# Performance work log

Measured on AMD Instinct MI355X. Metric: run time of the kernel, lower is better.

Reference implementation:

```python
import jax, jax.numpy as jnp
import numpy as np

NUM_HEADS = 16
EMBED_DIM = 2048
HEAD_DIM = EMBED_DIM // NUM_HEADS        # 128
LATENT_DIM = HEAD_DIM // 4               # 32
GROUPS = HEAD_DIM // LATENT_DIM          # 4 latent sub-heads per q head
B, T = 1, 2048


def setup_inputs() -> dict:
    key = jax.random.key(0)
    ks = jax.random.split(key, 7)
    s_in = 1.0 / np.sqrt(EMBED_DIM)
    x = jax.random.normal(ks[0], (B, T, EMBED_DIM), dtype=jnp.float32)
    # torch Linear weights: [out_features, in_features]
    Wq = jax.random.normal(ks[1], (EMBED_DIM, EMBED_DIM), dtype=jnp.float32) * s_in
    Wk = jax.random.normal(ks[2], (EMBED_DIM, EMBED_DIM), dtype=jnp.float32) * s_in
    Wv = jax.random.normal(ks[3], (EMBED_DIM, EMBED_DIM), dtype=jnp.float32) * s_in
    Wlk = jax.random.normal(ks[4], (NUM_HEADS * LATENT_DIM, EMBED_DIM), dtype=jnp.float32) * s_in
    Wlv = jax.random.normal(ks[5], (NUM_HEADS * LATENT_DIM, EMBED_DIM), dtype=jnp.float32) * s_in
    Wo = jax.random.normal(ks[6], (EMBED_DIM, EMBED_DIM), dtype=jnp.float32) * s_in
    return {"x": x, "Wq": Wq, "Wk": Wk, "Wv": Wv, "Wlk": Wlk, "Wlv": Wlv, "Wo": Wo}


def reference(x, Wq, Wk, Wv, Wlk, Wlv, Wo):
    Bv, Tv, C = x.shape
    # q: [B,T,H,G,Dl]  (each head's 128-dim q split into 4 latent sub-heads)
    q = (x @ Wq.T).reshape(Bv, Tv, NUM_HEADS, GROUPS, LATENT_DIM)
    # latent k/v: [B,T,H,Dl], shared across the G sub-heads of each q head
    lk = (x @ Wlk.T).reshape(Bv, Tv, NUM_HEADS, LATENT_DIM)
    lv = (x @ Wlv.T).reshape(Bv, Tv, NUM_HEADS, LATENT_DIM)
    # k_proj / v_proj outputs are computed but unused in the original forward.
    scale = 1.0 / np.sqrt(HEAD_DIM).astype(np.float32)
    # scores: [B,H,G,T,T]
    scores = jnp.einsum('bthgd,bshd->bhgts', q, lk) * scale
    probs = jax.nn.softmax(scores, axis=-1)
    out = jnp.einsum('bhgts,bshd->bthgd', probs, lv).reshape(Bv, Tv, C)
    return out @ Wo.T
```

## Files before the change

kernel.cpp:

```cpp
#include <hip/hip_runtime.h>
#include <hip/hip_bf16.h>

typedef __bf16 bf16;
typedef __bf16 bf16x4 __attribute__((ext_vector_type(4)));
typedef __bf16 bf16x8 __attribute__((ext_vector_type(8)));
typedef float  f32x4  __attribute__((ext_vector_type(4)));

#define AS1 __attribute__((address_space(1)))
#define AS3 __attribute__((address_space(3)))

__device__ __forceinline__ void gload_lds16(const bf16* g, bf16* l) {
    __builtin_amdgcn_global_load_lds((const AS1 void*)g, (AS3 void*)l, 16, 0, 0);
}

__device__ __forceinline__ void stage8_f32(const float* s, bf16* l) {
    float4 a = *(const float4*)s;
    float4 b = *(const float4*)(s + 4);
    bf16x8 o;
    o[0] = (bf16)a.x; o[1] = (bf16)a.y; o[2] = (bf16)a.z; o[3] = (bf16)a.w;
    o[4] = (bf16)b.x; o[5] = (bf16)b.y; o[6] = (bf16)b.z; o[7] = (bf16)b.w;
    *(bf16x8*)l = o;
}

template <bool AF32, bool BF32>
__device__ __forceinline__ void gemm_core64(
    const void* __restrict__ Av, const void* __restrict__ Bv,
    int m0, int n0, int K, f32x4 (&acc)[2][4],
    int wm, int r16, int q8)
{
    constexpr int LDA = AF32 ? 40 : 32;
    constexpr int LDB = BF32 ? 40 : 32;
    __shared__ __align__(16) bf16 As[2][128 * LDA];
    __shared__ __align__(16) bf16 Bs[2][64 * LDB];

    const int tid = threadIdx.x;
    const int i0 = tid, i1 = tid + 256;
    const int rA0 = i0 >> 2, rA1 = i1 >> 2;
    const int rB  = tid >> 2;
    const int c0  = (tid & 3) * 8;
    const size_t a0 = (size_t)(m0 + rA0) * K + c0;
    const size_t a1 = (size_t)(m0 + rA1) * K + c0;
    const size_t b0 = (size_t)(n0 + rB)  * K + c0;

    auto stage = [&](int buf, int k0) {
        if constexpr (AF32) {
            stage8_f32((const float*)Av + a0 + k0, &As[buf][rA0 * LDA + c0]);
            stage8_f32((const float*)Av + a1 + k0, &As[buf][rA1 * LDA + c0]);
        } else {
            gload_lds16((const bf16*)Av + a0 + k0, &As[buf][i0 * 8]);
            gload_lds16((const bf16*)Av + a1 + k0, &As[buf][i1 * 8]);
        }
        if constexpr (BF32) {
            stage8_f32((const float*)Bv + b0 + k0, &Bs[buf][rB * LDB + c0]);
        } else {
            gload_lds16((const bf16*)Bv + b0 + k0, &Bs[buf][tid * 8]);
        }
    };

    stage(0, 0);
    __syncthreads();

    int cur = 0;
    for (int k0 = 0; k0 < K; k0 += 32) {
        if (k0 + 32 < K) stage(cur ^ 1, k0 + 32);

        bf16x8 a[2], b[4];
#pragma unroll
        for (int r = 0; r < 2; ++r)
            a[r] = *(const bf16x8*)&As[cur][(wm + r * 16 + r16) * LDA + q8 * 8];
#pragma unroll
        for (int c = 0; c < 4; ++c)
            b[c] = *(const bf16x8*)&Bs[cur][(c * 16 + r16) * LDB + q8 * 8];
#pragma unroll
        for (int r = 0; r < 2; ++r)
#pragma unroll
            for (int c = 0; c < 4; ++c)
                acc[r][c] = __builtin_amdgcn_mfma_f32_16x16x32_bf16(a[r], b[c], acc[r][c], 0, 0, 0);

        asm volatile("s_waitcnt vmcnt(0) lgkmcnt(0)" ::: "memory");
        __builtin_amdgcn_s_barrier();
        __builtin_amdgcn_sched_barrier(0);
        cur ^= 1;
    }
}

__global__ __launch_bounds__(256) void cvt5(
    const float* __restrict__ s0, const float* __restrict__ s1,
    const float* __restrict__ s2, const float* __restrict__ s3,
    const float* __restrict__ s4,
    bf16* __restrict__ d0, bf16* __restrict__ d1, bf16* __restrict__ d2,
    bf16* __restrict__ d3, bf16* __restrict__ d4)
{
    const float* S[5] = {s0, s1, s2, s3, s4};
    bf16*        D[5] = {d0, d1, d2, d3, d4};
    const int    N[5] = {4194304, 4194304, 1048576, 1048576, 4194304};
    int y = blockIdx.y;
    int base = (blockIdx.x * 256 + threadIdx.x) * 8;
    if (base >= N[y]) return;
    stage8_f32(S[y] + base, D[y] + base);
}

template <bool F32>
__global__ __launch_bounds__(256) void proj_kernel_t(
    const void* __restrict__ x, const void* __restrict__ Wq,
    const void* __restrict__ Wlk, const void* __restrict__ Wlv,
    bf16* __restrict__ Q, bf16* __restrict__ LK, bf16* __restrict__ LVt)
{
    const int bx = blockIdx.x, by = blockIdx.y;
    const int tid = threadIdx.x, lane = tid & 63, wave = tid >> 6;
    const int wm = wave * 32;
    const int r16 = lane & 15, q8 = lane >> 4;
    f32x4 acc[2][4] = {};

    const void* Bv; int n0;
    if (bx < 32)      { Bv = Wq;  n0 = bx * 64; }
    else if (bx < 40) { Bv = Wlk; n0 = (bx - 32) * 64; }
    else              { Bv = Wlv; n0 = (bx - 40) * 64; }

    gemm_core64<F32, F32>(x, Bv, by * 128, n0, 2048, acc, wm, r16, q8);

    if (bx < 40) {
        bf16* C  = (bx < 32) ? Q : LK;
        int ldc  = (bx < 32) ? 2048 : 512;
        const float sc = (bx < 32) ? 0.08838834764831845f * 1.4426950408889634f : 1.0f;
#pragma unroll
        for (int r = 0; r < 2; ++r)
#pragma unroll
            for (int c = 0; c < 4; ++c)
#pragma unroll
                for (int i = 0; i < 4; ++i) {
                    int row = by * 128 + wm + r * 16 + q8 * 4 + i;
                    int col = n0 + c * 16 + r16;
                    C[(size_t)row * ldc + col] = (bf16)(acc[r][c][i] * sc);
                }
    } else {
#pragma unroll
        for (int r = 0; r < 2; ++r)
#pragma unroll
            for (int c = 0; c < 4; ++c) {
                int hd = n0 + c * 16 + r16;
                int tb = by * 128 + wm + r * 16 + q8 * 4;
                bf16x4 pk;
#pragma unroll
                for (int i = 0; i < 4; ++i) pk[i] = (bf16)acc[r][c][i];
                *(bf16x4*)&LVt[(size_t)hd * 2048 + tb] = pk;
            }
    }
}

template <bool BF32>
__global__ __launch_bounds__(256) void out_kernel_t(
    const bf16* __restrict__ A, const void* __restrict__ Wo, float* __restrict__ C)
{
    const int tid = threadIdx.x, lane = tid & 63, wave = tid >> 6;
    const int wm = wave * 32;
    const int r16 = lane & 15, q8 = lane >> 4;
    f32x4 acc[2][4] = {};
    gemm_core64<false, BF32>(A, Wo, blockIdx.y * 128, blockIdx.x * 64, 2048, acc, wm, r16, q8);
#pragma unroll
    for (int r = 0; r < 2; ++r)
#pragma unroll
        for (int c = 0; c < 4; ++c)
#pragma unroll
            for (int i = 0; i < 4; ++i) {
                int row = blockIdx.y * 128 + wm + r * 16 + q8 * 4 + i;
                int col = blockIdx.x * 64 + c * 16 + r16;
                C[(size_t)row * 2048 + col] = acc[r][c][i];
            }
}

__global__ __launch_bounds__(256, 4) void attn6(
    const bf16* __restrict__ Q, const bf16* __restrict__ LK,
    const bf16* __restrict__ LVt, bf16* __restrict__ O)
{
    __shared__ __align__(16) bf16 Ks[2][64 * 32];
    __shared__ __align__(16) bf16 Vs[2][32 * 64];
    __shared__ __align__(16) bf16 Ps[128 * 64];

    const int tid  = threadIdx.x;
    const int lane = tid & 63;
    const int w    = tid >> 6;
    const int r16  = lane & 15;
    const int q8   = lane >> 4;
    const int hg = blockIdx.y, h = hg >> 2, g = hg & 3;
    const int t0 = blockIdx.x * 128;

    bf16x8 qb[2];
#pragma unroll
    for (int p = 0; p < 2; ++p)
        qb[p] = *(const bf16x8*)(Q + (size_t)(t0 + w * 32 + p * 16 + r16) * 2048
                                 + h * 128 + g * 32 + q8 * 8);

    const int kr = tid >> 2;
    const int kq = (tid & 3) ^ ((tid >> 3) & 3);
    const bf16* kg = LK + (size_t)kr * 512 + h * 32 + kq * 8;
    const int vd = tid >> 3;
    const int vq = (tid & 7) ^ ((tid >> 3) & 7);
    const bf16* vg = LVt + (size_t)(h * 32 + vd) * 2048 + vq * 8;

    const int ksw = (r16 >> 1) & 3;
    const int vsw = r16 & 7;

    const int pk7 = r16 & 7;
    const int ph  = q8 >> 1;
    const int plo = (q8 & 1) * 4;
    const int pb0 = ((w * 2 + 0) * 16 + r16) * 64;
    const int pb1 = ((w * 2 + 1) * 16 + r16) * 64;

    bf16x8 ones;
#pragma unroll
    for (int j = 0; j < 8; ++j) ones[j] = (bf16)1.0f;

    f32x4 o_acc[2][2] = {};
    f32x4 l_acc[2] = {};
    const f32x4 z = {0.f, 0.f, 0.f, 0.f};

    gload_lds16(kg, &Ks[0][tid * 8]);
    gload_lds16(vg, &Vs[0][tid * 8]);
    __syncthreads();

    int cur = 0;
    for (int sb = 0; sb < 2048; sb += 64) {
        if (sb + 64 < 2048) {
            gload_lds16(kg + (size_t)(sb + 64) * 512, &Ks[cur ^ 1][tid * 8]);
            gload_lds16(vg + (sb + 64),               &Vs[cur ^ 1][tid * 8]);
        }
        const bf16* ks = Ks[cur];
        const bf16* vs = Vs[cur];

        bf16x8 kb[4], vb[2][2];
#pragma unroll
        for (int c = 0; c < 4; ++c)
            kb[c] = *(const bf16x8*)&ks[(c * 16 + r16) * 32 + (q8 ^ ksw) * 8];
#pragma unroll
        for (int kk = 0; kk < 2; ++kk)
#pragma unroll
            for (int ct = 0; ct < 2; ++ct)
                vb[kk][ct] = *(const bf16x8*)&vs[(ct * 16 + r16) * 64
                                                 + (((kk * 4 + q8) ^ vsw) * 8)];

#pragma unroll
        for (int p = 0; p < 2; ++p) {
            const int pbase = p ? pb1 : pb0;
            f32x4 s[4];
            __builtin_amdgcn_s_setprio(1);
#pragma unroll
            for (int c = 0; c < 4; ++c)
                s[c] = __builtin_amdgcn_mfma_f32_16x16x32_bf16(kb[c], qb[p], z, 0, 0, 0);
            __builtin_amdgcn_s_setprio(0);
#pragma unroll
            for (int c = 0; c < 4; ++c) {
                bf16x4 pkv;
#pragma unroll
                for (int i = 0; i < 4; ++i) pkv[i] = (bf16)exp2f(s[c][i]);
                *(bf16x4*)&Ps[pbase + ((c * 2 + ph) ^ pk7) * 8 + plo] = pkv;
            }
        }

        __builtin_amdgcn_s_setprio(1);
#pragma unroll
        for (int p = 0; p < 2; ++p) {
            const int pbase = p ? pb1 : pb0;
#pragma unroll
            for (int kk = 0; kk < 2; ++kk) {
                bf16x8 ap = *(const bf16x8*)&Ps[pbase + ((kk * 4 + q8) ^ pk7) * 8];
#pragma unroll
                for (int ct = 0; ct < 2; ++ct)
                    o_acc[p][ct] = __builtin_amdgcn_mfma_f32_16x16x32_bf16(ap, vb[kk][ct], o_acc[p][ct], 0, 0, 0);
                l_acc[p] = __builtin_amdgcn_mfma_f32_16x16x32_bf16(ap, ones, l_acc[p], 0, 0, 0);
            }
        }
        __builtin_amdgcn_s_setprio(0);

        asm volatile("s_waitcnt vmcnt(0) lgkmcnt(0)" ::: "memory");
        __builtin_amdgcn_s_barrier();
        __builtin_amdgcn_sched_barrier(0);
        cur ^= 1;
    }

#pragma unroll
    for (int p = 0; p < 2; ++p)
#pragma unroll
        for (int i = 0; i < 4; ++i) {
            float inv = 1.0f / l_acc[p][i];
            int t = t0 + w * 32 + p * 16 + q8 * 4 + i;
#pragma unroll
            for (int ct = 0; ct < 2; ++ct) {
                int d = ct * 16 + r16;
                O[(size_t)t * 2048 + h * 128 + g * 32 + d] = (bf16)(o_acc[p][ct][i] * inv);
            }
        }
}

extern "C" void kernel_launch(void* const* d_in, const int* in_sizes, int n_in,
                              void* d_out, int out_size, void* d_ws, size_t ws_size,
                              hipStream_t stream) {
    const float* x   = (const float*)d_in[0];
    const float* Wq  = (const float*)d_in[1];
    const float* Wlk = (const float*)d_in[4];
    const float* Wlv = (const float*)d_in[5];
    const float* Wo  = (const float*)d_in[6];
    float* out = (float*)d_out;

    const size_t M4 = 4194304, M1 = 1048576;
    const size_t need_fast = (M1 + M1 + M4 + M4 + M1 + M1) * 2;

    if (ws_size >= need_fast) {
        bf16* xb   = (bf16*)d_out;
        bf16* Wqb  = xb + M4;
        bf16* p    = (bf16*)d_ws;
        bf16* Wlkb = p; p += M1;
        bf16* Wlvb = p; p += M1;
        bf16* Wob  = p; p += M4;
        bf16* Qp   = p; p += M4;
        bf16* LKp  = p; p += M1;
        bf16* LVt  = p;
        bf16* ATT  = Qp;

        cvt5<<<dim3(2048, 5), 256, 0, stream>>>(x, Wq, Wlk, Wlv, Wo,
                                                xb, Wqb, Wlkb, Wlvb, Wob);
        proj_kernel_t<false><<<dim3(48, 16), 256, 0, stream>>>(xb, Wqb, Wlkb, Wlvb,
                                                               Qp, LKp, LVt);
        attn6<<<dim3(16, 64), 256, 0, stream>>>(Qp, LKp, LVt, ATT);
        out_kernel_t<false><<<dim3(32, 16), 256, 0, stream>>>(ATT, Wob, out);
    } else {
        bf16* Qp  = (bf16*)d_ws;
        bf16* LKp = Qp + M4;
        bf16* LVt = LKp + M1;
        bf16* ATT = Qp;

        proj_kernel_t<true><<<dim3(48, 16), 256, 0, stream>>>(x, Wq, Wlk, Wlv,
                                                              Qp, LKp, LVt);
        attn6<<<dim3(16, 64), 256, 0, stream>>>(Qp, LKp, LVt, ATT);
        out_kernel_t<true><<<dim3(32, 16), 256, 0, stream>>>(ATT, Wo, out);
    }
}
```

Before: 284.6 us.

## Use K=64 tiles with XOR-swizzled LDS for bf16 GEMM paths

Splits the shared GEMM core into an fp32-staging variant and a new bf16 variant. The bf16 variant stages 64-wide K tiles through direct global-to-LDS loads with an XOR swizzle on the column chunk. This halves the number of barrier-synchronised iterations and avoids LDS bank conflicts on the fragment reads. It costs more LDS per block, which may reduce occupancy, and the mixed bf16/fp32 output path is now duplicated inline.

```diff
diff --git a/kernel.cpp b/kernel.cpp
--- a/kernel.cpp
+++ b/kernel.cpp
@@ -22,20 +22,18 @@
     *(bf16x8*)l = o;
 }
 
-template <bool AF32, bool BF32>
-__device__ __forceinline__ void gemm_core64(
-    const void* __restrict__ Av, const void* __restrict__ Bv,
+__device__ __forceinline__ void gemm_core64_f32(
+    const float* __restrict__ Av, const float* __restrict__ Bv,
     int m0, int n0, int K, f32x4 (&acc)[2][4],
     int wm, int r16, int q8)
 {
-    constexpr int LDA = AF32 ? 40 : 32;
-    constexpr int LDB = BF32 ? 40 : 32;
+    constexpr int LDA = 40;
+    constexpr int LDB = 40;
     __shared__ __align__(16) bf16 As[2][128 * LDA];
     __shared__ __align__(16) bf16 Bs[2][64 * LDB];
 
     const int tid = threadIdx.x;
-    const int i0 = tid, i1 = tid + 256;
-    const int rA0 = i0 >> 2, rA1 = i1 >> 2;
+    const int rA0 = tid >> 2, rA1 = (tid + 256) >> 2;
     const int rB  = tid >> 2;
     const int c0  = (tid & 3) * 8;
     const size_t a0 = (size_t)(m0 + rA0) * K + c0;
@@ -43,18 +41,9 @@
     const size_t b0 = (size_t)(n0 + rB)  * K + c0;
 
     auto stage = [&](int buf, int k0) {
-        if constexpr (AF32) {
-            stage8_f32((const float*)Av + a0 + k0, &As[buf][rA0 * LDA + c0]);
-            stage8_f32((const float*)Av + a1 + k0, &As[buf][rA1 * LDA + c0]);
-        } else {
-            gload_lds16((const bf16*)Av + a0 + k0, &As[buf][i0 * 8]);
-            gload_lds16((const bf16*)Av + a1 + k0, &As[buf][i1 * 8]);
-        }
-        if constexpr (BF32) {
-            stage8_f32((const float*)Bv + b0 + k0, &Bs[buf][rB * LDB + c0]);
-        } else {
-            gload_lds16((const bf16*)Bv + b0 + k0, &Bs[buf][tid * 8]);
-        }
+        stage8_f32(Av + a0 + k0, &As[buf][rA0 * LDA + c0]);
+        stage8_f32(Av + a1 + k0, &As[buf][rA1 * LDA + c0]);
+        stage8_f32(Bv + b0 + k0, &Bs[buf][rB * LDB + c0]);
     };
 
     stage(0, 0);
@@ -76,6 +65,65 @@
 #pragma unroll
             for (int c = 0; c < 4; ++c)
                 acc[r][c] = __builtin_amdgcn_mfma_f32_16x16x32_bf16(a[r], b[c], acc[r][c], 0, 0, 0);
+
+        asm volatile("s_waitcnt vmcnt(0) lgkmcnt(0)" ::: "memory");
+        __builtin_amdgcn_s_barrier();
+        __builtin_amdgcn_sched_barrier(0);
+        cur ^= 1;
+    }
+}
+
+__device__ __forceinline__ void gemm_core64_k64(
+    const bf16* __restrict__ A, const bf16* __restrict__ B,
+    int m0, int n0, int K, f32x4 (&acc)[2][4],
+    int wm, int r16, int q8)
+{
+    __shared__ __align__(16) bf16 As[2][128 * 64];
+    __shared__ __align__(16) bf16 Bs[2][64 * 64];
+
+    const int tid  = threadIdx.x;
+    const int arow = tid >> 3;
+    const int acol = ((tid & 7) ^ ((tid >> 3) & 7)) * 8;
+    const int k7   = r16 & 7;
+
+    auto stage = [&](int buf, int kt) {
+#pragma unroll
+        for (int j = 0; j < 4; ++j)
+            gload_lds16(A + (size_t)(m0 + j * 32 + arow) * K + kt + acol,
+                        &As[buf][(j * 256 + tid) * 8]);
+#pragma unroll
+        for (int j = 0; j < 2; ++j)
+            gload_lds16(B + (size_t)(n0 + j * 32 + arow) * K + kt + acol,
+                        &Bs[buf][(j * 256 + tid) * 8]);
+    };
+
+    stage(0, 0);
+    __syncthreads();
+
+    int cur = 0;
+    for (int kt = 0; kt < K; kt += 64) {
+        if (kt + 64 < K) stage(cur ^ 1, kt + 64);
+
+        bf16x8 a[2][2], b[4][2];
+#pragma unroll
+        for (int r = 0; r < 2; ++r)
+#pragma unroll
+            for (int kc = 0; kc < 2; ++kc)
+                a[r][kc] = *(const bf16x8*)&As[cur][(wm + r * 16 + r16) * 64
+                                                   + ((kc * 4 + q8) ^ k7) * 8];
+#pragma unroll
+        for (int c = 0; c < 4; ++c)
+#pragma unroll
+            for (int kc = 0; kc < 2; ++kc)
+                b[c][kc] = *(const bf16x8*)&Bs[cur][(c * 16 + r16) * 64
+                                                   + ((kc * 4 + q8) ^ k7) * 8];
+#pragma unroll
+        for (int kc = 0; kc < 2; ++kc)
+#pragma unroll
+            for (int r = 0; r < 2; ++r)
+#pragma unroll
+                for (int c = 0; c < 4; ++c)
+                    acc[r][c] = __builtin_amdgcn_mfma_f32_16x16x32_bf16(a[r][kc], b[c][kc], acc[r][c], 0, 0, 0);
 
         asm volatile("s_waitcnt vmcnt(0) lgkmcnt(0)" ::: "memory");
         __builtin_amdgcn_s_barrier();
@@ -117,7 +165,10 @@
     else if (bx < 40) { Bv = Wlk; n0 = (bx - 32) * 64; }
     else              { Bv = Wlv; n0 = (bx - 40) * 64; }
 
-    gemm_core64<F32, F32>(x, Bv, by * 128, n0, 2048, acc, wm, r16, q8);
+    if constexpr (F32)
+        gemm_core64_f32((const float*)x, (const float*)Bv, by * 128, n0, 2048, acc, wm, r16, q8);
+    else
+        gemm_core64_k64((const bf16*)x, (const bf16*)Bv, by * 128, n0, 2048, acc, wm, r16, q8);
 
     if (bx < 40) {
         bf16* C  = (bx < 32) ? Q : LK;
@@ -156,7 +207,48 @@
     const int wm = wave * 32;
     const int r16 = lane & 15, q8 = lane >> 4;
     f32x4 acc[2][4] = {};
-    gemm_core64<false, BF32>(A, Wo, blockIdx.y * 128, blockIdx.x * 64, 2048, acc, wm, r16, q8);
+    if constexpr (BF32) {
+        __shared__ int dummy; (void)dummy;
+    }
+    if constexpr (!BF32)
+        gemm_core64_k64(A, (const bf16*)Wo, blockIdx.y * 128, blockIdx.x * 64, 2048, acc, wm, r16, q8);
+    else {
+        constexpr int LDA = 32, LDB = 40;
+        __shared__ __align__(16) bf16 As[2][128 * LDA];
+        __shared__ __align__(16) bf16 Bs[2][64 * LDB];
+        const int i0 = tid, i1 = tid + 256;
+        const int rB = tid >> 2, c0 = (tid & 3) * 8;
+        const size_t a0 = (size_t)(blockIdx.y * 128 + (i0 >> 2)) * 2048 + c0;
+        const size_t a1 = (size_t)(blockIdx.y * 128 + (i1 >> 2)) * 2048 + c0;
+        const size_t b0 = (size_t)(blockIdx.x * 64 + rB) * 2048 + c0;
+        auto stage = [&](int buf, int k0) {
+            gload_lds16(A + a0 + k0, &As[buf][i0 * 8]);
+            gload_lds16(A + a1 + k0, &As[buf][i1 * 8]);
+            stage8_f32((const float*)Wo + b0 + k0, &Bs[buf][rB * LDB + c0]);
+        };
+        stage(0, 0);
+        __syncthreads();
+        int cur = 0;
+        for (int k0 = 0; k0 < 2048; k0 += 32) {
+            if (k0 + 32 < 2048) stage(cur ^ 1, k0 + 32);
+            bf16x8 a[2], b[4];
+#pragma unroll
+            for (int r = 0; r < 2; ++r)
+                a[r] = *(const bf16x8*)&As[cur][(wm + r * 16 + r16) * LDA + q8 * 8];
+#pragma unroll
+            for (int c = 0; c < 4; ++c)
+                b[c] = *(const bf16x8*)&Bs[cur][(c * 16 + r16) * LDB + q8 * 8];
+#pragma unroll
+            for (int r = 0; r < 2; ++r)
+#pragma unroll
+                for (int c = 0; c < 4; ++c)
+                    acc[r][c] = __builtin_amdgcn_mfma_f32_16x16x32_bf16(a[r], b[c], acc[r][c], 0, 0, 0);
+            asm volatile("s_waitcnt vmcnt(0) lgkmcnt(0)" ::: "memory");
+            __builtin_amdgcn_s_barrier();
+            __builtin_amdgcn_sched_barrier(0);
+            cur ^= 1;
+        }
+    }
 #pragma unroll
     for (int r = 0; r < 2; ++r)
 #pragma unroll
```

Result: faster. 267.0 us (-6.2%).
